# Kernel optimization log

Measured on AMD Instinct MI355X. Metric: run time of the kernel, lower is better.

## Reference

```python
import jax, jax.numpy as jnp
import numpy as np

B, S, E, H = 2, 2048, 1024, 16
D = E // H  # head dim = 64
MAX_REL = 512


def setup_inputs() -> dict:
    key = jax.random.key(0)
    ks = jax.random.split(key, 12)
    w = 1.0 / np.sqrt(E)
    return {
        "query": jax.random.normal(ks[0], (B, S, E), jnp.float32),
        "key": jax.random.normal(ks[1], (B, S, E), jnp.float32),
        "value": jax.random.normal(ks[2], (B, S, E), jnp.float32),
        "Wq": jax.random.normal(ks[3], (E, E), jnp.float32) * w,
        "bq": jax.random.normal(ks[4], (E,), jnp.float32) * 0.02,
        "Wk": jax.random.normal(ks[5], (E, E), jnp.float32) * w,
        "bk": jax.random.normal(ks[6], (E,), jnp.float32) * 0.02,
        "Wv": jax.random.normal(ks[7], (E, E), jnp.float32) * w,
        "bv": jax.random.normal(ks[8], (E,), jnp.float32) * 0.02,
        "Wo": jax.random.normal(ks[9], (E, E), jnp.float32) * w,
        "bo": jax.random.normal(ks[10], (E,), jnp.float32) * 0.02,
        "rel_bias_table": jax.random.normal(ks[11], (2 * MAX_REL + 1, H), jnp.float32),
    }


def _rel_bias(rel_bias_table, sq, sk):
    # clamped relative positions -> [Sq, Sk] indices into table
    rel = jnp.arange(sq)[:, None] - jnp.arange(sk)[None, :]
    rel = jnp.clip(rel, -MAX_REL, MAX_REL) + MAX_REL
    bias = rel_bias_table[rel]                 # [Sq, Sk, H]
    return jnp.transpose(bias, (2, 0, 1))[None]  # [1, H, Sq, Sk]


def reference(query, key, value, Wq, bq, Wk, bk, Wv, bv, Wo, bo, rel_bias_table):
    b, sq, e = query.shape
    sk = key.shape[1]
    scale = D ** -0.5
    # projections (torch Linear: x @ W.T + b), split heads -> [B, H, S, D]
    q = (query @ Wq.T + bq).reshape(b, sq, H, D).transpose(0, 2, 1, 3)
    k = (key @ Wk.T + bk).reshape(b, sk, H, D).transpose(0, 2, 1, 3)
    v = (value @ Wv.T + bv).reshape(b, sk, H, D).transpose(0, 2, 1, 3)
    scores = jnp.einsum("bhqd,bhkd->bhqk", q, k) * scale
    scores = scores + _rel_bias(rel_bias_table, sq, sk)
    # causal mask (causal_mask=True branch)
    causal = jnp.arange(sk)[None, :] > jnp.arange(sq)[:, None]
    scores = jnp.where(causal[None, None], -jnp.inf, scores)
    attn = jax.nn.softmax(scores, axis=-1)
    out = jnp.einsum("bhqk,bhkd->bhqd", attn, v)
    out = out.transpose(0, 2, 1, 3).reshape(b, sq, e)
    out = out @ Wo.T + bo
    return out, attn
```

## Files before the change

### kernel.cpp

```cpp
#include <hip/hip_runtime.h>
#include <hip/hip_bf16.h>
#include <stdint.h>

#define Sx 2048
#define Ex 1024
#define Hx 16
#define Dx 64

typedef __attribute__((ext_vector_type(8))) short short8;
typedef __attribute__((ext_vector_type(4))) short bh4;
typedef __attribute__((ext_vector_type(4))) float f32x4;
typedef __attribute__((ext_vector_type(2))) unsigned int u32x2;

__device__ inline short f2bf(float f) {
    unsigned u = __builtin_bit_cast(unsigned, f);
    u = (u + 0x7fffu + ((u >> 16) & 1u)) >> 16;
    return (short)u;
}

__device__ inline unsigned cvtpk_bf16(float a, float b) {
    unsigned r;
    asm("v_cvt_pk_bf16_f32 %0, %1, %2" : "=v"(r) : "v"(a), "v"(b));
    return r;
}

__device__ inline float exp2fast(float x) { return __builtin_amdgcn_exp2f(x); }

__device__ inline void gload16(const short* g, short* l) {
    __builtin_amdgcn_global_load_lds((const __attribute__((address_space(1))) void*)g,
                                     (__attribute__((address_space(3))) void*)l, 16, 0, 0);
}

__global__ __launch_bounds__(256) void prep(const float* __restrict__ q,
                                            const float* __restrict__ k,
                                            const float* __restrict__ v,
                                            const float* __restrict__ wq,
                                            const float* __restrict__ wk,
                                            const float* __restrict__ wv_,
                                            const float* __restrict__ wo,
                                            short* __restrict__ ws) {
    const int seg = blockIdx.y;
    const float* src; size_t n, doff;
    switch (seg) {
        case 0: src = q;   n = 4194304; doff = 0;        break;
        case 1: src = k;   n = 4194304; doff = 4194304;  break;
        case 2: src = v;   n = 4194304; doff = 8388608;  break;
        case 3: src = wq;  n = 1048576; doff = 12582912; break;
        case 4: src = wk;  n = 1048576; doff = 13631488; break;
        case 5: src = wv_; n = 1048576; doff = 14680064; break;
        default: src = wo; n = 1048576; doff = 15728640; break;
    }
    short* dst = ws + doff;
    for (size_t i = ((size_t)blockIdx.x * 256 + threadIdx.x) * 8; i < n;
         i += (size_t)gridDim.x * 256 * 8) {
        float4 f0 = *(const float4*)&src[i];
        float4 f1 = *(const float4*)&src[i + 4];
        short8 s;
        s[0]=f2bf(f0.x); s[1]=f2bf(f0.y); s[2]=f2bf(f0.z); s[3]=f2bf(f0.w);
        s[4]=f2bf(f1.x); s[5]=f2bf(f1.y); s[6]=f2bf(f1.z); s[7]=f2bf(f1.w);
        *(short8*)&dst[i] = s;
    }
}

__global__ __launch_bounds__(256) void gemm_qkv3(const short* __restrict__ wsb,
                                                 const float* __restrict__ bq,
                                                 const float* __restrict__ bk,
                                                 const float* __restrict__ bv,
                                                 short* __restrict__ qh,
                                                 short* __restrict__ kh,
                                                 short* __restrict__ vt) {
    __shared__ short wt[128 * 64];
    __shared__ short xt[128 * 64];
    const int z = blockIdx.z;
    const short* X  = wsb + (size_t)z * 4194304;
    const short* Wm = wsb + 12582912 + (size_t)z * 1048576;
    const float* bias = (z == 0) ? bq : (z == 1) ? bk : bv;
    short* outb = (z == 0) ? qh : (z == 1) ? kh : vt;
    const bool vmode = (z == 2);

    const int tid = threadIdx.x;
    const int l = tid & 63, wv = tid >> 6;
    const int r15 = l & 15, g = l >> 4;
    const int wm = wv >> 1, wn = wv & 1;
    const int i0 = blockIdx.x << 7;
    const int j0 = blockIdx.y << 7;
    const int lrow = l >> 3, lgi = l & 7;

    f32x4 acc[4][4] = {};

    for (int k0 = 0; k0 < Ex; k0 += 64) {
        __syncthreads();
        #pragma unroll
        for (int p = 0; p < 4; ++p) {
            int row = p * 32 + wv * 8 + lrow;
            int col = ((lgi ^ (row & 7)) << 3) + k0;
            gload16(&Wm[(size_t)(j0 + row) * Ex + col], &wt[(p * 32 + wv * 8) * 64]);
            gload16(&X [(size_t)(i0 + row) * Ex + col], &xt[(p * 32 + wv * 8) * 64]);
        }
        __syncthreads();
        const short* At = vmode ? xt : wt;
        const short* Bt = vmode ? wt : xt;
        #pragma unroll
        for (int kk = 0; kk < 64; kk += 32) {
            const int sw = (((kk >> 3) + g) ^ (r15 & 7)) << 3;
            short8 a[4], b[4];
            #pragma unroll
            for (int m = 0; m < 4; ++m)
                a[m] = *(const short8*)&At[(wm * 64 + m * 16 + r15) * 64 + sw];
            #pragma unroll
            for (int n = 0; n < 4; ++n)
                b[n] = *(const short8*)&Bt[(wn * 64 + n * 16 + r15) * 64 + sw];
            #pragma unroll
            for (int m = 0; m < 4; ++m)
                #pragma unroll
                for (int n = 0; n < 4; ++n)
                    acc[m][n] = __builtin_amdgcn_mfma_f32_16x16x32_bf16(a[m], b[n], acc[m][n], 0, 0, 0);
        }
    }

    if (!vmode) {
        #pragma unroll
        for (int m = 0; m < 4; ++m) {
            int jb = j0 + wm * 64 + m * 16 + (g << 2);
            float4 bvv = *(const float4*)&bias[jb];
            #pragma unroll
            for (int n = 0; n < 4; ++n) {
                int i = i0 + wn * 64 + n * 16 + r15;
                bh4 s;
                s[0] = f2bf(acc[m][n][0] + bvv.x);
                s[1] = f2bf(acc[m][n][1] + bvv.y);
                s[2] = f2bf(acc[m][n][2] + bvv.z);
                s[3] = f2bf(acc[m][n][3] + bvv.w);
                *(bh4*)&outb[(size_t)i * Ex + jb] = s;
            }
        }
    } else {
        #pragma unroll
        for (int m = 0; m < 4; ++m) {
            int ib = i0 + wm * 64 + m * 16 + (g << 2);
            int b_ = ib >> 11, s0 = ib & 2047;
            #pragma unroll
            for (int n = 0; n < 4; ++n) {
                int j = j0 + wn * 64 + n * 16 + r15;
                float bj = bias[j];
                bh4 s;
                s[0] = f2bf(acc[m][n][0] + bj);
                s[1] = f2bf(acc[m][n][1] + bj);
                s[2] = f2bf(acc[m][n][2] + bj);
                s[3] = f2bf(acc[m][n][3] + bj);
                *(bh4*)&outb[((size_t)(b_ * Hx + (j >> 6)) * Dx + (j & 63)) * Sx + s0] = s;
            }
        }
    }
}

__global__ __launch_bounds__(256) void gemm_out(const short* __restrict__ Xb,
                                                const short* __restrict__ Wb,
                                                const float* __restrict__ bias,
                                                float* __restrict__ out) {
    __shared__ short wt[2][128 * 64];
    __shared__ short xt[2][128 * 64];
    const int tid = threadIdx.x;
    const int l = tid & 63, wv = tid >> 6;
    const int r15 = l & 15, g = l >> 4;
    const int wm = wv >> 1, wn = wv & 1;
    const int i0 = blockIdx.x << 7;
    const int j0 = blockIdx.y << 7;
    const int lrow = l >> 3, lgi = l & 7;

    f32x4 acc[4][4] = {};

    auto stage = [&](int it, int buf) {
        int k0 = it << 6;
        #pragma unroll
        for (int p = 0; p < 4; ++p) {
            int row = p * 32 + wv * 8 + lrow;
            int col = ((lgi ^ (row & 7)) << 3) + k0;
            gload16(&Wb[(size_t)(j0 + row) * Ex + col], &wt[buf][(p * 32 + wv * 8) * 64]);
            gload16(&Xb[(size_t)(i0 + row) * Ex + col], &xt[buf][(p * 32 + wv * 8) * 64]);
        }
    };

    stage(0, 0);
    for (int it = 0; it < 16; ++it) {
        __syncthreads();
        if (it + 1 < 16) stage(it + 1, (it + 1) & 1);
        const int cur = it & 1;
        #pragma unroll
        for (int kk = 0; kk < 64; kk += 32) {
            const int sw = (((kk >> 3) + g) ^ (r15 & 7)) << 3;
            short8 a[4], b[4];
            #pragma unroll
            for (int m = 0; m < 4; ++m)
                a[m] = *(const short8*)&wt[cur][(wm * 64 + m * 16 + r15) * 64 + sw];
            #pragma unroll
            for (int n = 0; n < 4; ++n)
                b[n] = *(const short8*)&xt[cur][(wn * 64 + n * 16 + r15) * 64 + sw];
            #pragma unroll
            for (int m = 0; m < 4; ++m)
                #pragma unroll
                for (int n = 0; n < 4; ++n)
                    acc[m][n] = __builtin_amdgcn_mfma_f32_16x16x32_bf16(a[m], b[n], acc[m][n], 0, 0, 0);
        }
    }

    #pragma unroll
    for (int m = 0; m < 4; ++m) {
        int jb = j0 + wm * 64 + m * 16 + (g << 2);
        float4 bvv = *(const float4*)&bias[jb];
        #pragma unroll
        for (int n = 0; n < 4; ++n) {
            int i = i0 + wn * 64 + n * 16 + r15;
            float4 o;
            o.x = acc[m][n][0] + bvv.x;
            o.y = acc[m][n][1] + bvv.y;
            o.z = acc[m][n][2] + bvv.z;
            o.w = acc[m][n][3] + bvv.w;
            *(float4*)&out[(size_t)i * Ex + jb] = o;
        }
    }
}

__global__ void attn_fused(const short* __restrict__ qhat,
                           const short* __restrict__ khat,
                           const short* __restrict__ vT,
                           const float* __restrict__ table,
                           float* __restrict__ attn,
                           short* __restrict__ om) {
    __shared__ short ks[2][64 * 64];
    __shared__ short vs[2][64 * 64];
    __shared__ short ps[2][128 * 64];
    __shared__ float bl[1028];

    const int tid = threadIdx.x;
    const int l = tid & 63, wv = tid >> 6;
    const int r15 = l & 15, g = l >> 4;

    const int lin = blockIdx.x + (blockIdx.y << 4);
    const int xcd = lin & 7, slot = lin >> 3;
    const int bh = xcd + ((slot & 3) << 3);
    const int qidx = (slot >> 2) & 7;
    const int qt = (slot >> 5) ? (15 - qidx) : qidx;

    const int b = bh >> 4, h = bh & 15;
    const int lrow = l >> 3, lgi = l & 7;
    const int nkt = 2 * qt + 2;
    const float cs2 = 0.18033688f;

    for (int i = tid; i < 1025; i += 512)
        bl[i] = (i < 512) ? -3e30f : (table[i * Hx + h] - 16.0f) * 1.4426950408889634f;

    short8 qf[2];
    {
        const size_t qrow = (size_t)(b * Sx + (qt << 7) + wv * 16 + r15);
        #pragma unroll
        for (int kk = 0; kk < 2; ++kk)
            qf[kk] = *(const short8*)&qhat[qrow * Ex + h * Dx + kk * 32 + g * 8];
    }

    auto stageK = [&](int kt, int buf) {
        int row = wv * 8 + lrow;
        gload16(&khat[(size_t)(b * Sx + (kt << 6) + row) * Ex + h * Dx + ((lgi ^ (row & 7)) << 3)],
                &ks[buf][(wv * 8) * 64]);
    };
    auto stageV = [&](int kt, int buf) {
        int row = wv * 8 + lrow;
        gload16(&vT[((size_t)bh * Dx + row) * Sx + (kt << 6) + ((lgi ^ (row & 7)) << 3)],
                &vs[buf][(wv * 8) * 64]);
    };

    float sr = 0.f;
    const int qg0 = (qt << 7) + wv * 16 + r15;

    stageK(0, 0);
    for (int kt = 0; kt < nkt; ++kt) {
        __syncthreads();
        if (kt + 1 < nkt) stageK(kt + 1, (kt + 1) & 1);
        const short* kb = ks[kt & 1];
        f32x4 sf[4] = {};
        __builtin_amdgcn_s_setprio(1);
        #pragma unroll
        for (int kk = 0; kk < 64; kk += 32) {
            const int sw = (((kk >> 3) + g) ^ (r15 & 7)) << 3;
            short8 a[4];
            #pragma unroll
            for (int m = 0; m < 4; ++m) a[m] = *(const short8*)&kb[(m * 16 + r15) * 64 + sw];
            #pragma unroll
            for (int m = 0; m < 4; ++m)
                sf[m] = __builtin_amdgcn_mfma_f32_16x16x32_bf16(a[m], qf[kk >> 5], sf[m], 0, 0, 0);
        }
        __builtin_amdgcn_s_setprio(0);
        const int kcb = (kt << 6) + (g << 2);
        int base = qg0 + 512 - kcb;
        float psum = 0.f;
        #pragma unroll
        for (int m = 0; m < 4; ++m) {
            int b0 = base - m * 16;
            #pragma unroll
            for (int r = 0; r < 4; ++r) {
                int idx = b0 - r;
                idx = idx > 1024 ? 1024 : idx;
                psum += exp2fast(fmaf(sf[m][r], cs2, bl[idx]));
            }
        }
        psum += __shfl_xor(psum, 16);
        psum += __shfl_xor(psum, 32);
        sr += psum;
    }

    const float inv = 1.0f / sr;
    f32x4 of[4] = {};
    float* Ap = attn + (size_t)bh * ((size_t)Sx * Sx);

    auto bulk_store = [&](int t) {
        const short* pb = ps[t & 1];
        const int j2 = tid & 15;
        int row = tid >> 4;
        #pragma unroll
        for (int h2 = 0; h2 < 4; ++h2, row += 32) {
            bh4 v = *(const bh4*)&pb[row * 64 + (((j2 >> 1) ^ (row & 7)) << 3) + (j2 & 1) * 4];
            f32x4 o;
            #pragma unroll
            for (int r = 0; r < 4; ++r)
                o[r] = __builtin_bit_cast(float, (unsigned)((unsigned short)v[r]) << 16);
            __builtin_nontemporal_store(o, (f32x4*)&Ap[(size_t)((qt << 7) + row) * Sx + (t << 6) + j2 * 4]);
        }
    };

    __syncthreads();
    stageK(0, 0); stageV(0, 0);
    for (int kt = 0; kt < nkt; ++kt) {
        __syncthreads();
        if (kt + 1 < nkt) { stageK(kt + 1, (kt + 1) & 1); stageV(kt + 1, (kt + 1) & 1); }
        if (kt > 0) bulk_store(kt - 1);
        const int cur = kt & 1;
        f32x4 sf[4] = {};
        __builtin_amdgcn_s_setprio(1);
        #pragma unroll
        for (int kk = 0; kk < 64; kk += 32) {
            const int sw = (((kk >> 3) + g) ^ (r15 & 7)) << 3;
            short8 a[4];
            #pragma unroll
            for (int m = 0; m < 4; ++m) a[m] = *(const short8*)&ks[cur][(m * 16 + r15) * 64 + sw];
            #pragma unroll
            for (int m = 0; m < 4; ++m)
                sf[m] = __builtin_amdgcn_mfma_f32_16x16x32_bf16(a[m], qf[kk >> 5], sf[m], 0, 0, 0);
        }
        __builtin_amdgcn_s_setprio(0);
        {
            const int qrow = wv * 16 + r15;
            short* pw = ps[cur];
            #pragma unroll
            for (int m = 0; m < 4; ++m) {
                int kc0 = (kt << 6) + m * 16 + (g << 2);
                int b0 = qg0 + 512 - kc0;
                float pv0, pv1, pv2, pv3;
                {
                    int i0_ = b0;     i0_ = i0_ > 1024 ? 1024 : i0_;
                    int i1_ = b0 - 1; i1_ = i1_ > 1024 ? 1024 : i1_;
                    int i2_ = b0 - 2; i2_ = i2_ > 1024 ? 1024 : i2_;
                    int i3_ = b0 - 3; i3_ = i3_ > 1024 ? 1024 : i3_;
                    pv0 = exp2fast(fmaf(sf[m][0], cs2, bl[i0_])) * inv;
                    pv1 = exp2fast(fmaf(sf[m][1], cs2, bl[i1_])) * inv;
                    pv2 = exp2fast(fmaf(sf[m][2], cs2, bl[i2_])) * inv;
                    pv3 = exp2fast(fmaf(sf[m][3], cs2, bl[i3_])) * inv;
                }
                u32x2 pk;
                pk[0] = cvtpk_bf16(pv0, pv1);
                pk[1] = cvtpk_bf16(pv2, pv3);
                int gphys = (m * 2 + (g >> 1)) ^ (r15 & 7);
                *(u32x2*)&pw[qrow * 64 + gphys * 8 + (g & 1) * 4] = pk;
            }
        }
        __builtin_amdgcn_s_setprio(1);
        #pragma unroll
        for (int kk = 0; kk < 64; kk += 32) {
            const int sw = (((kk >> 3) + g) ^ (r15 & 7)) << 3;
            short8 a[4], bp;
            #pragma unroll
            for (int m = 0; m < 4; ++m) a[m] = *(const short8*)&vs[cur][(m * 16 + r15) * 64 + sw];
            bp = *(const short8*)&ps[cur][(wv * 16 + r15) * 64 + sw];
            #pragma unroll
            for (int m = 0; m < 4; ++m)
                of[m] = __builtin_amdgcn_mfma_f32_16x16x32_bf16(a[m], bp, of[m], 0, 0, 0);
        }
        __builtin_amdgcn_s_setprio(0);
    }
    __syncthreads();
    bulk_store(nkt - 1);

    {
        const int qv = (qt << 7) + wv * 16 + r15;
        #pragma unroll
        for (int m = 0; m < 4; ++m) {
            int d0 = m * 16 + (g << 2);
            u32x2 s;
            s[0] = cvtpk_bf16(of[m][0], of[m][1]);
            s[1] = cvtpk_bf16(of[m][2], of[m][3]);
            *(u32x2*)&om[(size_t)(b * Sx + qv) * Ex + h * Dx + d0] = s;
        }
    }

    const int c0 = nkt << 6;
    f32x4 z = {0.f, 0.f, 0.f, 0.f};
    for (int row = tid >> 3; row < 128; row += 64) {
        size_t base = (size_t)((qt << 7) + row) * Sx;
        for (int c = c0 + ((tid & 7) << 2); c < Sx; c += 32)
            __builtin_nontemporal_store(z, (f32x4*)&Ap[base + c]);
    }
}

extern "C" void kernel_launch(void* const* d_in, const int* in_sizes, int n_in,
                              void* d_out, int out_size, void* d_ws, size_t ws_size,
                              hipStream_t stream) {
    const float* query = (const float*)d_in[0];
    const float* key   = (const float*)d_in[1];
    const float* value = (const float*)d_in[2];
    const float* bq = (const float*)d_in[4];
    const float* bk = (const float*)d_in[6];
    const float* bv = (const float*)d_in[8];
    const float* bo = (const float*)d_in[10];
    const float* Wq = (const float*)d_in[3];
    const float* Wk = (const float*)d_in[5];
    const float* Wv = (const float*)d_in[7];
    const float* Wo = (const float*)d_in[9];
    const float* tbl = (const float*)d_in[11];

    short* ws = (short*)d_ws;
    short* qx  = ws;
    short* wob = ws + 15728640;
    short* qh  = ws + 16777216;
    short* kh  = ws + 20971520;
    short* vt  = ws + 25165824;

    float* outp  = (float*)d_out;
    float* attnp = outp + 4194304;

    prep<<<dim3(1024, 7), 256, 0, stream>>>(query, key, value, Wq, Wk, Wv, Wo, ws);
    gemm_qkv3<<<dim3(32, 8, 3), 256, 0, stream>>>(ws, bq, bk, bv, qh, kh, vt);
    attn_fused<<<dim3(16, 32), 512, 0, stream>>>(qh, kh, vt, tbl, attnp, qx);
    gemm_out<<<dim3(32, 8), 256, 0, stream>>>(qx, wob, bo, outp);
}
```

Before: 224.0 us.

## Unify GEMMs into templated double-buffered kernel and split QKV launch

Replaces the single-buffered batched QKV projection GEMM with a templated double-buffered GEMM (the same one the output projection used) and issues Q, K and V as three separate launches. The aim is to overlap global-to-LDS loads with MFMA compute in the QKV projections and to resolve the mode at compile time. It doubles LDS use per block, which may reduce occupancy. Splitting into three launches of 256 blocks each also loses the larger 768-block grid and adds launch overhead.

Result: slower. 244.5 us (+9.1%).

```diff
diff --git a/kernel.cpp b/kernel.cpp
--- a/kernel.cpp
+++ b/kernel.cpp
@@ -62,22 +62,13 @@
     }
 }
 
-__global__ __launch_bounds__(256) void gemm_qkv3(const short* __restrict__ wsb,
-                                                 const float* __restrict__ bq,
-                                                 const float* __restrict__ bk,
-                                                 const float* __restrict__ bv,
-                                                 short* __restrict__ qh,
-                                                 short* __restrict__ kh,
-                                                 short* __restrict__ vt) {
-    __shared__ short wt[128 * 64];
-    __shared__ short xt[128 * 64];
-    const int z = blockIdx.z;
-    const short* X  = wsb + (size_t)z * 4194304;
-    const short* Wm = wsb + 12582912 + (size_t)z * 1048576;
-    const float* bias = (z == 0) ? bq : (z == 1) ? bk : bv;
-    short* outb = (z == 0) ? qh : (z == 1) ? kh : vt;
-    const bool vmode = (z == 2);
-
+template<int MODE>
+__global__ __launch_bounds__(256) void gemm128(const short* __restrict__ Xb,
+                                               const short* __restrict__ Wb,
+                                               const float* __restrict__ bias,
+                                               void* __restrict__ outp) {
+    __shared__ short wt[2][128 * 64];
+    __shared__ short xt[2][128 * 64];
     const int tid = threadIdx.x;
     const int l = tid & 63, wv = tid >> 6;
     const int r15 = l & 15, g = l >> 4;
@@ -88,18 +79,24 @@
 
     f32x4 acc[4][4] = {};
 
-    for (int k0 = 0; k0 < Ex; k0 += 64) {
-        __syncthreads();
+    auto stage = [&](int it, int buf) {
+        int k0 = it << 6;
         #pragma unroll
         for (int p = 0; p < 4; ++p) {
             int row = p * 32 + wv * 8 + lrow;
             int col = ((lgi ^ (row & 7)) << 3) + k0;
-            gload16(&Wm[(size_t)(j0 + row) * Ex + col], &wt[(p * 32 + wv * 8) * 64]);
-            gload16(&X [(size_t)(i0 + row) * Ex + col], &xt[(p * 32 + wv * 8) * 64]);
-        }
+            gload16(&Wb[(size_t)(j0 + row) * Ex + col], &wt[buf][(p * 32 + wv * 8) * 64]);
+            gload16(&Xb[(size_t)(i0 + row) * Ex + col], &xt[buf][(p * 32 + wv * 8) * 64]);
+        }
+    };
+
+    stage(0, 0);
+    for (int it = 0; it < 16; ++it) {
         __syncthreads();
-        const short* At = vmode ? xt : wt;
-        const short* Bt = vmode ? wt : xt;
+        if (it + 1 < 16) stage(it + 1, (it + 1) & 1);
+        const int cur = it & 1;
+        const short* At = (MODE == 1) ? xt[cur] : wt[cur];
+        const short* Bt = (MODE == 1) ? wt[cur] : xt[cur];
         #pragma unroll
         for (int kk = 0; kk < 64; kk += 32) {
             const int sw = (((kk >> 3) + g) ^ (r15 & 7)) << 3;
@@ -118,7 +115,8 @@
         }
     }
 
-    if (!vmode) {
+    if (MODE == 0) {
+        short* outb = (short*)outp;
         #pragma unroll
         for (int m = 0; m < 4; ++m) {
             int jb = j0 + wm * 64 + m * 16 + (g << 2);
@@ -134,7 +132,25 @@
                 *(bh4*)&outb[(size_t)i * Ex + jb] = s;
             }
         }
+    } else if (MODE == 2) {
+        float* outf = (float*)outp;
+        #pragma unroll
+        for (int m = 0; m < 4; ++m) {
+            int jb = j0 + wm * 64 + m * 16 + (g << 2);
+            float4 bvv = *(const float4*)&bias[jb];
+            #pragma unroll
+            for (int n = 0; n < 4; ++n) {
+                int i = i0 + wn * 64 + n * 16 + r15;
+                float4 o;
+                o.x = acc[m][n][0] + bvv.x;
+                o.y = acc[m][n][1] + bvv.y;
+                o.z = acc[m][n][2] + bvv.z;
+                o.w = acc[m][n][3] + bvv.w;
+                *(float4*)&outf[(size_t)i * Ex + jb] = o;
+            }
+        }
     } else {
+        short* outb = (short*)outp;
         #pragma unroll
         for (int m = 0; m < 4; ++m) {
             int ib = i0 + wm * 64 + m * 16 + (g << 2);
@@ -150,73 +166,6 @@
                 s[3] = f2bf(acc[m][n][3] + bj);
                 *(bh4*)&outb[((size_t)(b_ * Hx + (j >> 6)) * Dx + (j & 63)) * Sx + s0] = s;
             }
-        }
-    }
-}
-
-__global__ __launch_bounds__(256) void gemm_out(const short* __restrict__ Xb,
-                                                const short* __restrict__ Wb,
-                                                const float* __restrict__ bias,
-                                                float* __restrict__ out) {
-    __shared__ short wt[2][128 * 64];
-    __shared__ short xt[2][128 * 64];
-    const int tid = threadIdx.x;
-    const int l = tid & 63, wv = tid >> 6;
-    const int r15 = l & 15, g = l >> 4;
-    const int wm = wv >> 1, wn = wv & 1;
-    const int i0 = blockIdx.x << 7;
-    const int j0 = blockIdx.y << 7;
-    const int lrow = l >> 3, lgi = l & 7;
-
-    f32x4 acc[4][4] = {};
-
-    auto stage = [&](int it, int buf) {
-        int k0 = it << 6;
-        #pragma unroll
-        for (int p = 0; p < 4; ++p) {
-            int row = p * 32 + wv * 8 + lrow;
-            int col = ((lgi ^ (row & 7)) << 3) + k0;
-            gload16(&Wb[(size_t)(j0 + row) * Ex + col], &wt[buf][(p * 32 + wv * 8) * 64]);
-            gload16(&Xb[(size_t)(i0 + row) * Ex + col], &xt[buf][(p * 32 + wv * 8) * 64]);
-        }
-    };
-
-    stage(0, 0);
-    for (int it = 0; it < 16; ++it) {
-        __syncthreads();
-        if (it + 1 < 16) stage(it + 1, (it + 1) & 1);
-        const int cur = it & 1;
-        #pragma unroll
-        for (int kk = 0; kk < 64; kk += 32) {
-            const int sw = (((kk >> 3) + g) ^ (r15 & 7)) << 3;
-            short8 a[4], b[4];
-            #pragma unroll
-            for (int m = 0; m < 4; ++m)
-                a[m] = *(const short8*)&wt[cur][(wm * 64 + m * 16 + r15) * 64 + sw];
-            #pragma unroll
-            for (int n = 0; n < 4; ++n)
-                b[n] = *(const short8*)&xt[cur][(wn * 64 + n * 16 + r15) * 64 + sw];
-            #pragma unroll
-            for (int m = 0; m < 4; ++m)
-                #pragma unroll
-                for (int n = 0; n < 4; ++n)
-                    acc[m][n] = __builtin_amdgcn_mfma_f32_16x16x32_bf16(a[m], b[n], acc[m][n], 0, 0, 0);
-        }
-    }
-
-    #pragma unroll
-    for (int m = 0; m < 4; ++m) {
-        int jb = j0 + wm * 64 + m * 16 + (g << 2);
-        float4 bvv = *(const float4*)&bias[jb];
-        #pragma unroll
-        for (int n = 0; n < 4; ++n) {
-            int i = i0 + wn * 64 + n * 16 + r15;
-            float4 o;
-            o.x = acc[m][n][0] + bvv.x;
-            o.y = acc[m][n][1] + bvv.y;
-            o.z = acc[m][n][2] + bvv.z;
-            o.w = acc[m][n][3] + bvv.w;
-            *(float4*)&out[(size_t)i * Ex + jb] = o;
         }
     }
 }
@@ -428,6 +377,11 @@
 
     short* ws = (short*)d_ws;
     short* qx  = ws;
+    short* kx  = ws + 4194304;
+    short* vx  = ws + 8388608;
+    short* wqb = ws + 12582912;
+    short* wkb = ws + 13631488;
+    short* wvb = ws + 14680064;
     short* wob = ws + 15728640;
     short* qh  = ws + 16777216;
     short* kh  = ws + 20971520;
@@ -436,8 +390,11 @@
     float* outp  = (float*)d_out;
     float* attnp = outp + 4194304;
 
+    dim3 g128(32, 8);
     prep<<<dim3(1024, 7), 256, 0, stream>>>(query, key, value, Wq, Wk, Wv, Wo, ws);
-    gemm_qkv3<<<dim3(32, 8, 3), 256, 0, stream>>>(ws, bq, bk, bv, qh, kh, vt);
+    gemm128<0><<<g128, 256, 0, stream>>>(qx, wqb, bq, qh);
+    gemm128<0><<<g128, 256, 0, stream>>>(kx, wkb, bk, kh);
+    gemm128<1><<<g128, 256, 0, stream>>>(vx, wvb, bv, vt);
     attn_fused<<<dim3(16, 32), 512, 0, stream>>>(qh, kh, vt, tbl, attnp, qx);
-    gemm_out<<<dim3(32, 8), 256, 0, stream>>>(qx, wob, bo, outp);
-}
+    gemm128<2><<<g128, 256, 0, stream>>>(qx, wob, bo, outp);
+}
```
